# Kernel tuning notes

Hardware: AMD Instinct MI355X
Metric: run time of the kernel (lower is better)

## Reference

```python
import jax, jax.numpy as jnp
import numpy as np

D = 512      # model_channels
H = 4        # heads
L = 4        # num_transfomers_layers
DK = D // H
EPS = 1e-5


def inorm(x):
    # nn.InstanceNorm1d(d_model) applied to (bs, seq, d_model): normalizes over
    # the last (d_model) axis per token, no affine params.
    m = jnp.mean(x, axis=-1, keepdims=True)
    v = jnp.var(x, axis=-1, keepdims=True)
    return (x - m) * jax.lax.rsqrt(v + EPS)


def mha(xq, xkv, w, b, mask):
    # w: [4, D, D] (q,k,v,out), b: [4, D]; mask: [bs,S,S] (1 = masked)
    bs, S, _ = xq.shape
    q = (xq @ w[0] + b[0]).reshape(bs, S, H, DK).transpose(0, 2, 1, 3)
    k = (xkv @ w[1] + b[1]).reshape(bs, S, H, DK).transpose(0, 2, 1, 3)
    v = (xkv @ w[2] + b[2]).reshape(bs, S, H, DK).transpose(0, 2, 1, 3)
    scores = jnp.einsum('bhqd,bhkd->bhqk', q, k) / jnp.sqrt(jnp.float32(DK))
    scores = jnp.where(mask[:, None] == 1, jnp.float32(-1e9), scores)
    attn = jax.nn.softmax(scores, axis=-1)
    out = jnp.einsum('bhqk,bhkd->bhqd', attn, v)
    out = out.transpose(0, 2, 1, 3).reshape(bs, S, D)
    return out @ w[3] + b[3]


def setup_inputs() -> dict:
    key = jax.random.key(0)
    ks = jax.random.split(key, 24)
    bs, S = 16, 512
    sc = 0.02
    inp = {
        'x': jax.random.normal(ks[0], (bs, S, 18), jnp.float32),
        'cond': jax.random.normal(ks[1], (bs, S, 89), jnp.float32),
        'door_mask': jax.random.randint(ks[2], (bs, S, S), 0, 2, jnp.int32),
        'self_mask': jax.random.randint(ks[3], (bs, S, S), 0, 2, jnp.int32),
        'gen_mask': jax.random.randint(ks[4], (bs, S, S), 0, 2, jnp.int32),
        # attention params: [L, 3 branches (door,self,gen), 4 projs (q,k,v,out)]
        'attn_w': jax.random.normal(ks[5], (L, 3, 4, D, D), jnp.float32) * sc,
        'attn_b': jnp.zeros((L, 3, 4, D), jnp.float32),
        'ff_w1': jax.random.normal(ks[6], (L, D, 2 * D), jnp.float32) * sc,
        'ff_b1': jnp.zeros((L, 2 * D), jnp.float32),
        'ff_w2': jax.random.normal(ks[7], (L, 2 * D, D), jnp.float32) * sc,
        'ff_b2': jnp.zeros((L, D), jnp.float32),
        'in_w': jax.random.normal(ks[8], (18, D), jnp.float32) * sc,
        'in_b': jnp.zeros((D,), jnp.float32),
        'cond_w': jax.random.normal(ks[9], (89, D), jnp.float32) * sc,
        'cond_b': jnp.zeros((D,), jnp.float32),
        'out1_w': jax.random.normal(ks[10], (D, D), jnp.float32) * sc,
        'out1_b': jnp.zeros((D,), jnp.float32),
        'out2_w': jax.random.normal(ks[11], (D, D // 2), jnp.float32) * sc,
        'out2_b': jnp.zeros((D // 2,), jnp.float32),
        'out3_w': jax.random.normal(ks[12], (D // 2, 2), jnp.float32) * sc,
        'out3_b': jnp.zeros((2,), jnp.float32),
    }
    return inp


def reference(x, cond, door_mask, self_mask, gen_mask,
              attn_w, attn_b, ff_w1, ff_b1, ff_w2, ff_b2,
              in_w, in_b, cond_w, cond_b,
              out1_w, out1_b, out2_w, out2_b, out3_w, out3_b):
    h = (x @ in_w + in_b) + (cond @ cond_w + cond_b)  # [bs,S,D]
    for l in range(L):
        h2 = inorm(h)
        h = (h
             + mha(h2, h2, attn_w[l, 0], attn_b[l, 0], door_mask)
             + mha(h2, h2, attn_w[l, 1], attn_b[l, 1], self_mask)
             + mha(h2, h2, attn_w[l, 2], attn_b[l, 2], gen_mask))
        h2 = inorm(h)
        h = h + jax.nn.relu(h2 @ ff_w1[l] + ff_b1[l]) @ ff_w2[l] + ff_b2[l]
    out = jax.nn.relu(h @ out1_w + out1_b)
    out = jax.nn.relu(out @ out2_w + out2_b)
    out = out @ out3_w + out3_b  # [bs,S,2]
    return out
```

## Files before the change

kernel.cpp:

```cpp
#include <hip/hip_runtime.h>
#include <hip/hip_bf16.h>

#define DEV static __device__ __forceinline__

typedef __attribute__((ext_vector_type(8))) short bfx8;
typedef __attribute__((ext_vector_type(4))) float f32x4;
typedef __attribute__((ext_vector_type(4))) unsigned short us4;

DEV unsigned short f2bf(float f){
  unsigned u = __builtin_bit_cast(unsigned, f);
  u += 0x7fffu + ((u >> 16) & 1u);
  return (unsigned short)(u >> 16);
}
DEV float bf2f(unsigned short h){
  unsigned u = ((unsigned)h) << 16;
  return __builtin_bit_cast(float, u);
}
DEV unsigned cvt_pk_bf16(float lo, float hi){
  unsigned r;
  asm("v_cvt_pk_bf16_f32 %0, %1, %2" : "=v"(r) : "v"(lo), "v"(hi));
  return r;
}
DEV void gld16(const void* g, void* l){
  __builtin_amdgcn_global_load_lds((const __attribute__((address_space(1))) void*)g,
                                   (__attribute__((address_space(3))) void*)l, 16, 0, 0);
}
DEV f32x4 mfma16(bfx8 a, bfx8 b, f32x4 c){
  return __builtin_amdgcn_mfma_f32_16x16x32_bf16(a, b, c, 0, 0, 0);
}

#define BAR() do{ asm volatile("" ::: "memory"); __builtin_amdgcn_s_barrier(); \
                  asm volatile("" ::: "memory"); }while(0)

__global__ __launch_bounds__(256, 2)
void wconv_kernel(const float* __restrict__ attn_w, const float* __restrict__ ff_w1,
                  const float* __restrict__ ff_w2, const float* __restrict__ out1_w,
                  const float* __restrict__ out2_w,
                  unsigned short* __restrict__ bqkv, unsigned short* __restrict__ bout,
                  unsigned short* __restrict__ bff1, unsigned short* __restrict__ bff2,
                  unsigned short* __restrict__ bo1, unsigned short* __restrict__ bo2)
{
  __shared__ float ts[64][65];
  const int z = blockIdx.z;
  const float* src; unsigned short* dst; int K, N, stride;
  if (z < 48){
    int l = z / 12, br = (z % 12) >> 2, p = z & 3;
    src = attn_w + (size_t)z * 262144; K = 512; N = 512;
    if (p < 3){ dst = bqkv + (size_t)l * 4608 * 512 + (size_t)(br * 3 + p) * 262144; stride = 512; }
    else      { dst = bout + (size_t)l * 512 * 1536 + (size_t)br * 512;              stride = 1536; }
  } else if (z < 52){
    int l = z - 48; src = ff_w1 + (size_t)l * 524288; K = 512; N = 1024;
    dst = bff1 + (size_t)l * 524288; stride = 512;
  } else if (z < 56){
    int l = z - 52; src = ff_w2 + (size_t)l * 524288; K = 1024; N = 512;
    dst = bff2 + (size_t)l * 524288; stride = 1024;
  } else if (z == 56){
    src = out1_w; K = 512; N = 512; dst = bo1; stride = 512;
  } else {
    src = out2_w; K = 512; N = 256; dst = bo2; stride = 512;
  }
  const int n0 = blockIdx.x << 6, k0 = blockIdx.y << 6;
  if (n0 >= N || k0 >= K) return;
  const int tx = threadIdx.x & 63, ty = threadIdx.x >> 6;
  #pragma unroll
  for (int i = 0; i < 16; ++i){
    int row = (ty << 4) + i;
    ts[row][tx] = src[(size_t)(k0 + row) * N + n0 + tx];
  }
  __syncthreads();
  #pragma unroll
  for (int i = 0; i < 16; ++i){
    int row = (ty << 4) + i;
    dst[(size_t)(n0 + row) * stride + k0 + tx] = f2bf(ts[tx][row]);
  }
}

__global__ __launch_bounds__(256, 4)
void mpack_kernel(const int* __restrict__ m0, const int* __restrict__ m1,
                  const int* __restrict__ m2, unsigned long long* __restrict__ mp)
{
  const int row = (blockIdx.x << 2) + (threadIdx.x >> 6);
  const int lane = threadIdx.x & 63;
  const int* src = (row < 8192) ? (m0 + (size_t)row * 512)
                 : (row < 16384 ? (m1 + (size_t)(row - 8192) * 512)
                                : (m2 + (size_t)(row - 16384) * 512));
  #pragma unroll
  for (int c = 0; c < 8; ++c){
    const int v = src[(c << 6) + lane];
    const unsigned long long b = __ballot(v != 0);
    if (lane == c) mp[(size_t)row * 8 + c] = b;
  }
}

__global__ __launch_bounds__(256, 4)
void embed_kernel(const float* __restrict__ x, const float* __restrict__ cond,
                  const float* __restrict__ in_w, const float* __restrict__ in_b,
                  const float* __restrict__ cond_w, const float* __restrict__ cond_b,
                  float* __restrict__ h)
{
  __shared__ float xs[8][18];
  __shared__ float cs[8][89];
  const int m0 = blockIdx.x << 3;
  const int tid = threadIdx.x;
  for (int i = tid; i < 144; i += 256) xs[i / 18][i % 18] = x[(size_t)m0 * 18 + i];
  for (int i = tid; i < 712; i += 256) cs[i / 89][i % 89] = cond[(size_t)m0 * 89 + i];
  __syncthreads();
  #pragma unroll
  for (int hf = 0; hf < 2; ++hf){
    const int c = tid + (hf << 8);
    const float bsum = in_b[c] + cond_b[c];
    float a[8];
    #pragma unroll
    for (int mi = 0; mi < 8; ++mi) a[mi] = bsum;
    #pragma unroll
    for (int k = 0; k < 18; ++k){
      const float wv = in_w[k * 512 + c];
      #pragma unroll
      for (int mi = 0; mi < 8; ++mi) a[mi] += xs[mi][k] * wv;
    }
    for (int k = 0; k < 89; ++k){
      const float wv = cond_w[k * 512 + c];
      #pragma unroll
      for (int mi = 0; mi < 8; ++mi) a[mi] += cs[mi][k] * wv;
    }
    #pragma unroll
    for (int mi = 0; mi < 8; ++mi) h[(size_t)(m0 + mi) * 512 + c] = a[mi];
  }
}

__global__ __launch_bounds__(256, 4)
void inorm_kernel(const float* __restrict__ in, unsigned short* __restrict__ ob)
{
  const int wid = (blockIdx.x << 2) + (threadIdx.x >> 6);
  const int lane = threadIdx.x & 63;
  const float* row = in + (size_t)wid * 512;
  const float4 v0 = *(const float4*)(row + (lane << 2));
  const float4 v1 = *(const float4*)(row + 256 + (lane << 2));
  float s = v0.x + v0.y + v0.z + v0.w + v1.x + v1.y + v1.z + v1.w;
  float q = v0.x*v0.x + v0.y*v0.y + v0.z*v0.z + v0.w*v0.w
          + v1.x*v1.x + v1.y*v1.y + v1.z*v1.z + v1.w*v1.w;
  #pragma unroll
  for (int sh = 1; sh < 64; sh <<= 1){
    s += __shfl_xor(s, sh, 64);
    q += __shfl_xor(q, sh, 64);
  }
  const float mean = s * (1.f / 512.f);
  const float var = q * (1.f / 512.f) - mean * mean;
  const float rs = rsqrtf(var + 1e-5f);
  us4 o0, o1;
  o0[0] = f2bf((v0.x - mean) * rs); o0[1] = f2bf((v0.y - mean) * rs);
  o0[2] = f2bf((v0.z - mean) * rs); o0[3] = f2bf((v0.w - mean) * rs);
  o1[0] = f2bf((v1.x - mean) * rs); o1[1] = f2bf((v1.y - mean) * rs);
  o1[2] = f2bf((v1.z - mean) * rs); o1[3] = f2bf((v1.w - mean) * rs);
  *(us4*)(ob + (size_t)wid * 512 + (lane << 2)) = o0;
  *(us4*)(ob + (size_t)wid * 512 + 256 + (lane << 2)) = o1;
}

__global__ void f2b_kernel(const float* __restrict__ in, unsigned short* __restrict__ ob, int n)
{
  const int i = (blockIdx.x * 256 + threadIdx.x) << 2;
  if (i >= n) return;
  const float4 v = *(const float4*)(in + i);
  us4 o; o[0] = f2bf(v.x); o[1] = f2bf(v.y); o[2] = f2bf(v.z); o[3] = f2bf(v.w);
  *(us4*)(ob + i) = o;
}

template<int MODE>
__global__ __launch_bounds__(256, 2)
void gemm_bt(const unsigned short* __restrict__ A, const unsigned short* __restrict__ B,
             const float* __restrict__ bias, float* __restrict__ Cf,
             unsigned short* __restrict__ Cb, unsigned short* __restrict__ qkp,
             unsigned short* __restrict__ vtp, int M, int N, int K)
{
  __shared__ unsigned short As[128 * 64];
  __shared__ unsigned short Bs[128 * 64];
  const int tid = threadIdx.x;
  const int w = tid >> 6, lane = tid & 63;
  const int wm = w >> 1, wn = w & 1;
  const int lr = lane & 15, lh = lane >> 4;
  const int m0 = blockIdx.x << 7, n0 = blockIdx.y << 7;
  const int rA = lane >> 3;
  const int cA = (lane & 7) << 3;

  f32x4 acc[4][4];
  #pragma unroll
  for (int i = 0; i < 4; ++i)
    #pragma unroll
    for (int j = 0; j < 4; ++j) acc[i][j] = (f32x4)0.f;

  const int nkt = K >> 6;
  auto stage = [&](int kt){
    #pragma unroll
    for (int c = 0; c < 4; ++c){
      const int r = (c << 5) + (w << 3) + rA;
      gld16(A + (size_t)(m0 + r) * K + (kt << 6) + cA,
            (char*)As + ((c << 5) + (w << 3)) * 128);
      gld16(B + (size_t)(n0 + r) * K + (kt << 6) + cA,
            (char*)Bs + ((c << 5) + (w << 3)) * 128);
    }
  };
  stage(0);
  for (int kt = 0; kt < nkt; ++kt){
    __syncthreads();
    #pragma unroll
    for (int kk = 0; kk < 2; ++kk){
      bfx8 af[4], bg[4];
      #pragma unroll
      for (int i = 0; i < 4; ++i)
        af[i] = *(const bfx8*)(As + ((wm << 6) + (i << 4) + lr) * 64 + (kk << 5) + (lh << 3));
      #pragma unroll
      for (int j = 0; j < 4; ++j)
        bg[j] = *(const bfx8*)(Bs + ((wn << 6) + (j << 4) + lr) * 64 + (kk << 5) + (lh << 3));
      #pragma unroll
      for (int i = 0; i < 4; ++i)
        #pragma unroll
        for (int j = 0; j < 4; ++j)
          acc[i][j] = mfma16(af[i], bg[j], acc[i][j]);
    }
    __syncthreads();
    if (kt + 1 < nkt) stage(kt + 1);
  }
  #pragma unroll
  for (int i = 0; i < 4; ++i){
    const int row = m0 + (wm << 6) + (i << 4) + (lh << 2);
    #pragma unroll
    for (int j = 0; j < 4; ++j){
      const int col = n0 + (wn << 6) + (j << 4) + lr;
      if constexpr (MODE == 1){
        const float bv = bias ? bias[col] : 0.f;
        #pragma unroll
        for (int r = 0; r < 4; ++r){
          float v = acc[i][j][r] + bv;
          v = fmaxf(v, 0.f);
          Cb[(size_t)(row + r) * N + col] = f2bf(v);
        }
      } else if constexpr (MODE == 2){
        const float bv = bias ? bias[col] : 0.f;
        #pragma unroll
        for (int r = 0; r < 4; ++r)
          Cf[(size_t)(row + r) * N + col] += acc[i][j][r] + bv;
      } else {
        const int br = col / 1536;
        const int rem = col - br * 1536;
        const int p = rem >> 9;
        const int c = rem & 511;
        const float bv = bias ? bias[(size_t)((br << 2) + p) * 512 + c] : 0.f;
        if (p < 2){
          #pragma unroll
          for (int r = 0; r < 4; ++r)
            qkp[((size_t)((br << 1) + p) * 8192 + row + r) * 512 + c] = f2bf(acc[i][j][r] + bv);
        } else {
          const int b_ = row >> 9, s0 = row & 511;
          const int hi = c >> 7, dk = c & 127;
          us4 pk;
          #pragma unroll
          for (int r = 0; r < 4; ++r) pk[r] = f2bf(acc[i][j][r] + bv);
          *(us4*)(vtp + (((size_t)(br * 16 + b_) * 4 + hi) * 128 + dk) * 512 + s0) = pk;
        }
      }
    }
  }
}

__global__ __launch_bounds__(512, 4)
void attn_kernel(const unsigned short* __restrict__ qk, const unsigned short* __restrict__ vt,
                 const unsigned* __restrict__ mp, unsigned short* __restrict__ outp)
{
  __shared__ unsigned short KV[3][8192];
  __shared__ unsigned short Pl[8][16 * 40];
  __shared__ unsigned Mk[8][16 * 17];
  const int tid = threadIdx.x;
  const int w = tid >> 6, lane = tid & 63;
  const int lr = lane & 15, lh = lane >> 4;
  const int id = blockIdx.x;
  const int wg = (id & 7) * 96 + (id >> 3);
  const int qt = wg & 3, head = wg >> 2;
  const int br = head >> 6, bh = head & 63;
  const int b = bh >> 2, h = bh & 3;
  const int q0 = (qt << 7) + (w << 4);

  const unsigned short* qbase = qk + ((size_t)(br * 2 + 0) * 8192 + (size_t)b * 512) * 512 + h * 128;
  const unsigned short* kbase = qk + ((size_t)(br * 2 + 1) * 8192 + (size_t)b * 512) * 512 + h * 128;
  const unsigned short* vbase = vt + ((size_t)(br * 16 + b) * 4 + h) * 128 * 512;
  const unsigned* mrow = mp + ((size_t)br * 8192 + (size_t)b * 512 + q0) * 16;

  unsigned* mk = Mk[w];
  #pragma unroll
  for (int u = 0; u < 4; ++u){
    const int idx = (lane << 2) + u;
    const int rw = idx >> 4, wd = idx & 15;
    mk[rw * 17 + wd] = mrow[rw * 16 + wd];
  }
  asm volatile("s_waitcnt lgkmcnt(0)" ::: "memory");
  __builtin_amdgcn_sched_barrier(0);

  bfx8 aq[4];
  #pragma unroll
  for (int t = 0; t < 4; ++t)
    aq[t] = *(const bfx8*)(qbase + (size_t)(q0 + lr) * 512 + (t << 5) + (lh << 3));

  const int krow = (w << 2) + (lane >> 4);
  const int kg = (lane & 15) ^ (krow & 7);
  const int vrow = (w << 4) + (lane >> 2);
  const int vg = (lane & 3) ^ ((vrow & 3) ^ ((vrow >> 2) & 3));
  auto stageKt = [&](int kt, int buf){
    gld16(kbase + ((size_t)((kt << 5) + krow) << 9) + (kg << 3),
          (char*)&KV[buf][w << 9]);
    gld16(vbase + ((size_t)vrow << 9) + (kt << 5) + (vg << 3),
          (char*)&KV[buf][4096 + (w << 9)]);
  };

  const float scale = 0.08838834764831845f;
  f32x4 ao[8];
  #pragma unroll
  for (int j = 0; j < 8; ++j) ao[j] = (f32x4)0.f;
  float m = -3e38f;
  float lp = 0.f;
  unsigned short* pw = Pl[w];

  stageKt(0, 0); stageKt(1, 1);
  int bcur = 0;
  for (int kt = 0; kt < 16; ++kt){
    if (kt < 15) asm volatile("s_waitcnt vmcnt(2)" ::: "memory");
    else         asm volatile("s_waitcnt vmcnt(0)" ::: "memory");
    BAR();
    if (kt < 14){
      const int bst = (bcur == 0) ? 2 : bcur - 1;
      stageKt(kt + 2, bst);
    }
    const unsigned short* Kb = &KV[bcur][0];
    const unsigned short* Vb = &KV[bcur][4096];

    f32x4 st[2];
    const unsigned mword = mk[lr * 17 + kt];
    #pragma unroll
    for (int j = 0; j < 2; ++j){
      const int rk = (j << 4) + lr;
      f32x4 a2 = (f32x4)0.f;
      __builtin_amdgcn_s_setprio(1);
      #pragma unroll
      for (int t = 0; t < 4; ++t){
        const int s = ((t << 2) + lh) ^ (rk & 7);
        bfx8 bk = *(const bfx8*)&Kb[rk * 128 + (s << 3)];
        a2 = mfma16(bk, aq[t], a2);
      }
      __builtin_amdgcn_s_setprio(0);
      #pragma unroll
      for (int r = 0; r < 4; ++r){
        const int bit = (mword >> ((j << 4) + (lh << 2) + r)) & 1;
        st[j][r] = bit ? -1e9f : a2[r] * scale;
      }
    }

    float pmax = fmaxf(fmaxf(fmaxf(st[0][0], st[0][1]), fmaxf(st[0][2], st[0][3])),
                       fmaxf(fmaxf(st[1][0], st[1][1]), fmaxf(st[1][2], st[1][3])));
    pmax = fmaxf(pmax, __shfl_xor(pmax, 16, 64));
    pmax = fmaxf(pmax, __shfl_xor(pmax, 32, 64));
    if (__any(pmax > m + 8.f)){
      const float mn = fmaxf(m, pmax);
      const float f = __expf(m - mn);
      m = mn; lp *= f;
      float fr[4];
      #pragma unroll
      for (int r = 0; r < 4; ++r) fr[r] = __shfl(f, (lh << 2) + r, 64);
      #pragma unroll
      for (int j = 0; j < 8; ++j)
        #pragma unroll
        for (int r = 0; r < 4; ++r) ao[j][r] *= fr[r];
    }
    #pragma unroll
    for (int j = 0; j < 2; ++j){
      #pragma unroll
      for (int r = 0; r < 4; ++r){
        st[j][r] = __expf(st[j][r] - m);
        lp += st[j][r];
      }
      uint2 pk;
      pk.x = cvt_pk_bf16(st[j][0], st[j][1]);
      pk.y = cvt_pk_bf16(st[j][2], st[j][3]);
      *(uint2*)(pw + lr * 40 + (j << 4) + (lh << 2)) = pk;
    }
    asm volatile("s_waitcnt lgkmcnt(0)" ::: "memory");
    __builtin_amdgcn_sched_barrier(0);
    bfx8 pa = *(const bfx8*)(pw + lr * 40 + (lh << 3));

    __builtin_amdgcn_s_setprio(1);
    #pragma unroll
    for (int j = 0; j < 8; ++j){
      const int dd = (j << 4) + lr;
      const int s = lh ^ ((dd & 3) ^ ((dd >> 2) & 3));
      bfx8 bv = *(const bfx8*)&Vb[dd * 32 + (s << 3)];
      ao[j] = mfma16(pa, bv, ao[j]);
    }
    __builtin_amdgcn_s_setprio(0);
    asm volatile("" ::: "memory");
    bcur = (bcur == 2) ? 0 : bcur + 1;
  }

  lp += __shfl_xor(lp, 16, 64);
  lp += __shfl_xor(lp, 32, 64);
  const float rcp = 1.f / lp;
  float linv[4];
  #pragma unroll
  for (int r = 0; r < 4; ++r) linv[r] = __shfl(rcp, (lh << 2) + r, 64);
  const size_t obase = (size_t)(b * 512) * 1536 + br * 512 + h * 128;
  #pragma unroll
  for (int j = 0; j < 8; ++j){
    const int d = (j << 4) + lr;
    #pragma unroll
    for (int r = 0; r < 4; ++r){
      const int q = q0 + (lh << 2) + r;
      outp[obase + (size_t)q * 1536 + d] = f2bf(ao[j][r] * linv[r]);
    }
  }
}

__global__ __launch_bounds__(256, 4)
void out3_kernel(const unsigned short* __restrict__ t2, const float* __restrict__ w,
                 const float* __restrict__ b2, float* __restrict__ outp)
{
  const int row = (blockIdx.x << 2) + (threadIdx.x >> 6);
  const int lane = threadIdx.x & 63;
  const unsigned short* rp = t2 + (size_t)row * 256 + (lane << 2);
  float a0 = 0.f, a1 = 0.f;
  #pragma unroll
  for (int k = 0; k < 4; ++k){
    const float v = bf2f(rp[k]);
    const int kk = (lane << 2) + k;
    a0 += v * w[kk * 2 + 0];
    a1 += v * w[kk * 2 + 1];
  }
  #pragma unroll
  for (int s = 1; s < 64; s <<= 1){
    a0 += __shfl_xor(a0, s, 64);
    a1 += __shfl_xor(a1, s, 64);
  }
  if (lane == 0){
    outp[(size_t)row * 2 + 0] = a0 + b2[0];
    outp[(size_t)row * 2 + 1] = a1 + b2[1];
  }
}

extern "C" void kernel_launch(void* const* d_in, const int* in_sizes, int n_in,
                              void* d_out, int out_size, void* d_ws, size_t ws_size,
                              hipStream_t stream)
{
  const float* x      = (const float*)d_in[0];
  const float* cond   = (const float*)d_in[1];
  const int*   mdoor  = (const int*)d_in[2];
  const int*   mself  = (const int*)d_in[3];
  const int*   mgen   = (const int*)d_in[4];
  const float* attn_w = (const float*)d_in[5];
  const float* attn_b = (const float*)d_in[6];
  const float* ff_w1  = (const float*)d_in[7];
  const float* ff_b1  = (const float*)d_in[8];
  const float* ff_w2  = (const float*)d_in[9];
  const float* ff_b2  = (const float*)d_in[10];
  const float* in_w   = (const float*)d_in[11];
  const float* in_b   = (const float*)d_in[12];
  const float* cond_w = (const float*)d_in[13];
  const float* cond_b = (const float*)d_in[14];
  const float* out1_w = (const float*)d_in[15];
  const float* out1_b = (const float*)d_in[16];
  const float* out2_w = (const float*)d_in[17];
  const float* out2_b = (const float*)d_in[18];
  const float* out3_w = (const float*)d_in[19];
  const float* out3_b = (const float*)d_in[20];

  char* p = (char*)d_ws;
  auto carve = [&](size_t bytes) -> char* {
    char* r = p; p += (bytes + 255) & ~(size_t)255; return r;
  };
  float*          h    = (float*)carve(8192ull * 512 * 4);
  unsigned short* h2   = (unsigned short*)carve(8192ull * 512 * 2);
  unsigned short* bqkv = (unsigned short*)carve(4ull * 4608 * 512 * 2);
  unsigned short* bout = (unsigned short*)carve(4ull * 512 * 1536 * 2);
  unsigned short* bff1 = (unsigned short*)carve(4ull * 1024 * 512 * 2);
  unsigned short* bff2 = (unsigned short*)carve(4ull * 512 * 1024 * 2);
  unsigned short* bo1  = (unsigned short*)carve(512ull * 512 * 2);
  unsigned short* bo2  = (unsigned short*)carve(256ull * 512 * 2);
  unsigned short* qkb  = (unsigned short*)carve(6ull * 8192 * 512 * 2);
  unsigned short* vtb  = (unsigned short*)carve(3ull * 16 * 4 * 128 * 512 * 2);
  unsigned short* att  = (unsigned short*)carve(8192ull * 1536 * 2);
  unsigned short* t    = (unsigned short*)carve(8192ull * 1024 * 2);
  unsigned short* t2   = (unsigned short*)carve(8192ull * 256 * 2);
  unsigned long long* mpk = (unsigned long long*)carve(24576ull * 8 * 8);
  float* outf = (float*)d_out;

  wconv_kernel<<<dim3(16, 16, 58), 256, 0, stream>>>(attn_w, ff_w1, ff_w2, out1_w, out2_w,
                                                     bqkv, bout, bff1, bff2, bo1, bo2);
  mpack_kernel<<<dim3(6144), 256, 0, stream>>>(mdoor, mself, mgen, mpk);
  embed_kernel<<<dim3(1024), 256, 0, stream>>>(x, cond, in_w, in_b, cond_w, cond_b, h);
  for (int l = 0; l < 4; ++l){
    inorm_kernel<<<dim3(2048), 256, 0, stream>>>(h, h2);
    gemm_bt<3><<<dim3(64, 36), 256, 0, stream>>>(h2, bqkv + (size_t)l * 4608 * 512,
        attn_b + (size_t)l * 6144, nullptr, nullptr, qkb, vtb, 8192, 4608, 512);
    attn_kernel<<<dim3(768), 512, 0, stream>>>(qkb, vtb, (const unsigned*)mpk, att);
    gemm_bt<2><<<dim3(64, 4), 256, 0, stream>>>(att, bout + (size_t)l * 512 * 1536,
        nullptr, h, nullptr, nullptr, nullptr, 8192, 512, 1536);
    inorm_kernel<<<dim3(2048), 256, 0, stream>>>(h, h2);
    gemm_bt<1><<<dim3(64, 8), 256, 0, stream>>>(h2, bff1 + (size_t)l * 1024 * 512,
        ff_b1 + (size_t)l * 1024, nullptr, t, nullptr, nullptr, 8192, 1024, 512);
    gemm_bt<2><<<dim3(64, 4), 256, 0, stream>>>(t, bff2 + (size_t)l * 512 * 1024,
        ff_b2 + (size_t)l * 512, h, nullptr, nullptr, nullptr, 8192, 512, 1024);
  }
  f2b_kernel<<<dim3(4096), 256, 0, stream>>>(h, h2, 8192 * 512);
  gemm_bt<1><<<dim3(64, 4), 256, 0, stream>>>(h2, bo1, out1_b, nullptr, att, nullptr, nullptr, 8192, 512, 512);
  gemm_bt<1><<<dim3(64, 2), 256, 0, stream>>>(att, bo2, out2_b, nullptr, t2, nullptr, nullptr, 8192, 256, 512);
  out3_kernel<<<dim3(2048), 256, 0, stream>>>(t2, out3_w, out3_b, outf);
}
```

Baseline: 1.175 ms.

## Double-buffer GEMM LDS tiles with XOR swizzle and MFMA priority

The bf16 GEMM kernel now keeps two LDS buffers for A and B. It issues the global-to-LDS load for the next K tile before computing on the current one, using vmcnt waits so memory latency overlaps with MFMA work. Global source columns are XOR-swizzled by row and the fragment reads apply the matching swizzle, which is meant to reduce LDS bank conflicts. s_setprio raises wave priority around the MFMA block. Doubling LDS to 64KB per block may reduce occupancy relative to the launch_bounds target of 2 blocks.

After: 1.145 ms. 1.03x faster.

```diff
diff --git a/kernel.cpp b/kernel.cpp
--- a/kernel.cpp
+++ b/kernel.cpp
@@ -172,15 +172,15 @@
              unsigned short* __restrict__ Cb, unsigned short* __restrict__ qkp,
              unsigned short* __restrict__ vtp, int M, int N, int K)
 {
-  __shared__ unsigned short As[128 * 64];
-  __shared__ unsigned short Bs[128 * 64];
+  __shared__ unsigned short As[2][128 * 64];
+  __shared__ unsigned short Bs[2][128 * 64];
   const int tid = threadIdx.x;
   const int w = tid >> 6, lane = tid & 63;
   const int wm = w >> 1, wn = w & 1;
   const int lr = lane & 15, lh = lane >> 4;
   const int m0 = blockIdx.x << 7, n0 = blockIdx.y << 7;
   const int rA = lane >> 3;
-  const int cA = (lane & 7) << 3;
+  const int gsw = ((lane & 7) ^ rA) << 3;
 
   f32x4 acc[4][4];
   #pragma unroll
@@ -189,36 +189,48 @@
     for (int j = 0; j < 4; ++j) acc[i][j] = (f32x4)0.f;
 
   const int nkt = K >> 6;
-  auto stage = [&](int kt){
+  auto stage = [&](int kt, int buf){
     #pragma unroll
     for (int c = 0; c < 4; ++c){
       const int r = (c << 5) + (w << 3) + rA;
-      gld16(A + (size_t)(m0 + r) * K + (kt << 6) + cA,
-            (char*)As + ((c << 5) + (w << 3)) * 128);
-      gld16(B + (size_t)(n0 + r) * K + (kt << 6) + cA,
-            (char*)Bs + ((c << 5) + (w << 3)) * 128);
+      gld16(A + (size_t)(m0 + r) * K + (kt << 6) + gsw,
+            (char*)As[buf] + ((c << 5) + (w << 3)) * 128);
+      gld16(B + (size_t)(n0 + r) * K + (kt << 6) + gsw,
+            (char*)Bs[buf] + ((c << 5) + (w << 3)) * 128);
     }
   };
-  stage(0);
+  stage(0, 0);
   for (int kt = 0; kt < nkt; ++kt){
-    __syncthreads();
+    const int buf = kt & 1;
+    if (kt + 1 < nkt){
+      stage(kt + 1, buf ^ 1);
+      asm volatile("s_waitcnt vmcnt(8)" ::: "memory");
+    } else {
+      asm volatile("s_waitcnt vmcnt(0)" ::: "memory");
+    }
+    BAR();
     #pragma unroll
     for (int kk = 0; kk < 2; ++kk){
       bfx8 af[4], bg[4];
       #pragma unroll
-      for (int i = 0; i < 4; ++i)
-        af[i] = *(const bfx8*)(As + ((wm << 6) + (i << 4) + lr) * 64 + (kk << 5) + (lh << 3));
-      #pragma unroll
-      for (int j = 0; j < 4; ++j)
-        bg[j] = *(const bfx8*)(Bs + ((wn << 6) + (j << 4) + lr) * 64 + (kk << 5) + (lh << 3));
+      for (int i = 0; i < 4; ++i){
+        const int ra = (wm << 6) + (i << 4) + lr;
+        af[i] = *(const bfx8*)(As[buf] + ra * 64 + ((((kk << 2) + lh) ^ (lr & 7)) << 3));
+      }
+      #pragma unroll
+      for (int j = 0; j < 4; ++j){
+        const int rb = (wn << 6) + (j << 4) + lr;
+        bg[j] = *(const bfx8*)(Bs[buf] + rb * 64 + ((((kk << 2) + lh) ^ (lr & 7)) << 3));
+      }
+      __builtin_amdgcn_s_setprio(1);
       #pragma unroll
       for (int i = 0; i < 4; ++i)
         #pragma unroll
         for (int j = 0; j < 4; ++j)
           acc[i][j] = mfma16(af[i], bg[j], acc[i][j]);
-    }
-    __syncthreads();
-    if (kt + 1 < nkt) stage(kt + 1);
+      __builtin_amdgcn_s_setprio(0);
+    }
+    BAR();
   }
   #pragma unroll
   for (int i = 0; i < 4; ++i){
```
